# Kernel optimization log

Measured on AMD Instinct MI355X. Metric: run time of the kernel, lower is better.

The kernel has to match this reference:

```python
import jax, jax.numpy as jnp
import numpy as np

B, T, D = 2, 2048, 2048
H, L = 16, 64
Hd = D // H  # 128
SCALE = 1.0 / np.sqrt(L).astype(np.float32)


def apply_rope(q, k, freqs):
    # q, k: [B, T, H, Hd]; freqs: [T, Hd//2] angles (theta)
    cos = jnp.cos(freqs)[None, :, None, :]  # [1,T,1,Hd/2]
    sin = jnp.sin(freqs)[None, :, None, :]

    def rot(t):
        tr = t.reshape(*t.shape[:-1], Hd // 2, 2)
        a, b = tr[..., 0], tr[..., 1]
        return jnp.stack([a * cos - b * sin, a * sin + b * cos], axis=-1).reshape(t.shape)

    return rot(q), rot(k)


def setup_inputs() -> dict:
    key = jax.random.key(0)
    ks = jax.random.split(key, 16)

    def w(k, shape):
        return jax.random.normal(k, shape, jnp.float32) * 0.02

    x = jax.random.normal(ks[0], (B, T, D), jnp.float32)
    # RoPE angles: theta[t, i] = t / 10000^(2i/Hd)
    inv = 1.0 / (10000.0 ** (jnp.arange(0, Hd, 2, dtype=jnp.float32) / Hd))
    freqs = jnp.arange(T, dtype=jnp.float32)[:, None] * inv[None, :]  # [T, Hd/2]
    # additive causal mask
    mask = jnp.where(jnp.tril(jnp.ones((T, T), bool)), 0.0, -1e9).astype(jnp.float32)

    return dict(
        x=x, freqs=freqs, mask=mask,
        Wq=w(ks[1], (D, D)), bq=jnp.zeros((D,), jnp.float32),
        Wk=w(ks[2], (D, D)), bk=jnp.zeros((D,), jnp.float32),
        Wv=w(ks[3], (D, D)), bv=jnp.zeros((D,), jnp.float32),
        Wo=w(ks[4], (D, D)), bo=jnp.zeros((D,), jnp.float32),
        Wcq=w(ks[5], (Hd, L)), bcq=jnp.zeros((L,), jnp.float32),
        Wck=w(ks[6], (Hd, L)), bck=jnp.zeros((L,), jnp.float32),
        Wcv=w(ks[7], (Hd, L)), bcv=jnp.zeros((L,), jnp.float32),
        Wd=w(ks[8], (L, Hd)), bd=jnp.zeros((Hd,), jnp.float32),
    )


def reference(x, freqs, mask, Wq, bq, Wk, bk, Wv, bv, Wo, bo,
              Wcq, bcq, Wck, bck, Wcv, bcv, Wd, bd):
    b, t, d = x.shape
    q = (x @ Wq + bq).reshape(b, t, H, Hd)
    k = (x @ Wk + bk).reshape(b, t, H, Hd)
    v = (x @ Wv + bv).reshape(b, t, H, Hd)

    q, k = apply_rope(q, k, freqs)

    # per-head latent compression [B,T,H,L]
    q_lat = jnp.einsum('bthd,dl->bthl', q, Wcq) + bcq
    k_lat = jnp.einsum('bthd,dl->bthl', k, Wck) + bck
    v_lat = jnp.einsum('bthd,dl->bthl', v, Wcv) + bcv

    scores = jnp.einsum('bthl,bshl->bhts', q_lat, k_lat) * SCALE
    scores = scores + mask[None, None, :, :]
    attn = jax.nn.softmax(scores, axis=-1)

    out = jnp.einsum('bhts,bshl->bthl', attn, v_lat)  # [B,T,H,L]
    out = jnp.einsum('bthl,lk->bthk', out, Wd) + bd    # decompress -> [B,T,H,Hd]
    out = out.reshape(b, t, d)
    return out @ Wo + bo
```

## Files before the change

### kernel.cpp

```cpp
#include <hip/hip_runtime.h>
#include <hip/hip_bf16.h>

static constexpr int Bsz = 2;
static constexpr int Tn  = 2048;
static constexpr int Dn  = 2048;
static constexpr int Hn  = 16;
static constexpr int Ln  = 64;
static constexpr int Hd  = 128;
static constexpr float SL2E = 0.125f * 1.44269504088896f;

typedef short short8 __attribute__((ext_vector_type(8)));
typedef float f32x4 __attribute__((ext_vector_type(4)));
typedef unsigned short ushort8 __attribute__((ext_vector_type(8)));
typedef unsigned short ushort4v __attribute__((ext_vector_type(4)));
typedef _Float16 half8 __attribute__((ext_vector_type(8)));
typedef unsigned short u16;

__device__ inline u16 f16_rne(float f) {
  _Float16 h = (_Float16)f;
  union { _Float16 h; u16 u; } x; x.h = h;
  return x.u;
}
__device__ inline float f16_to_f(u16 u) {
  union { u16 u; _Float16 h; } x; x.u = u;
  return (float)x.h;
}

#define GL(g, l) __builtin_amdgcn_global_load_lds(                     \
    (const __attribute__((address_space(1))) void*)(g),                \
    (__attribute__((address_space(3))) void*)(l), 16, 0, 0)

__global__ void split_h(const float* __restrict__ A, u16* __restrict__ O,
                        int nblk, int Kd) {
  int b = blockIdx.x * 256 + threadIdx.x;
  if (b >= nblk) return;
  int perRow = Kd >> 3;
  int m = b / perRow, gb = b - m * perRow;
  int w = gb >> 2, g = gb & 3;
  const float* src = A + (size_t)m * Kd + (w << 5) + (g << 2);
  float4 v0 = *(const float4*)src;
  float4 v1 = *(const float4*)(src + 16);
  float e[8] = {v0.x, v0.y, v0.z, v0.w, v1.x, v1.y, v1.z, v1.w};
  ushort8 o;
#pragma unroll
  for (int j = 0; j < 8; ++j) o[j] = f16_rne(e[j]);
  *(ushort8*)(O + (size_t)b * 8) = o;
}

__global__ __launch_bounds__(256) void transpose_h2(
    const float* __restrict__ W0, const float* __restrict__ W1,
    u16* __restrict__ T0, u16* __restrict__ T1, int Kd, int Nd) {
  const float* W = blockIdx.z ? W1 : W0;
  u16* Th = blockIdx.z ? T1 : T0;
  __shared__ float t[32][33];
  int k0 = blockIdx.x * 32, n0 = blockIdx.y * 32;
  int i = threadIdx.x;
  {
    int kk = i >> 3, nn = (i & 7) << 2;
    float4 v = *(const float4*)&W[(size_t)(k0 + kk) * Nd + n0 + nn];
    t[kk][nn] = v.x; t[kk][nn + 1] = v.y; t[kk][nn + 2] = v.z; t[kk][nn + 3] = v.w;
  }
  __syncthreads();
  int n = i >> 3, t2 = i & 7;
  int g = t2 >> 1, h = t2 & 1;
  int kbase = h * 16 + g * 4;
  ushort4v o;
#pragma unroll
  for (int j = 0; j < 4; ++j) o[j] = f16_rne(t[kbase + j][n]);
  *(ushort4v*)(Th + (size_t)(n0 + n) * Kd + k0 + t2 * 4) = o;
}

__global__ __launch_bounds__(256) void fold64(
    const float* __restrict__ A, int lda, int a_bx, int a_by,
    const float* __restrict__ B, int ldb, int b_bx, int b_by,
    float* __restrict__ C, int ldc, int c_bx, int c_by) {
  __shared__ float a_lds[64][132];
  __shared__ float b_lds[128][64];
  const int bx = blockIdx.x, by = blockIdx.y, tid = threadIdx.x;
  A += (size_t)bx * a_bx + (size_t)by * a_by;
  B += (size_t)bx * b_bx + (size_t)by * b_by;
  C += (size_t)bx * c_bx + (size_t)by * c_by;
  for (int i = tid; i < 64 * 32; i += 256) {
    int r = i >> 5, c4 = (i & 31) << 2;
    *(float4*)&a_lds[r][c4] = *(const float4*)&A[(size_t)r * lda + c4];
  }
  for (int i = tid; i < 128 * 16; i += 256) {
    int r = i >> 4, c4 = (i & 15) << 2;
    *(float4*)&b_lds[r][c4] = *(const float4*)&B[(size_t)r * ldb + c4];
  }
  __syncthreads();
  const int r = tid >> 2, l0 = (tid & 3) << 4;
  float acc[16] = {};
  for (int k = 0; k < 128; ++k) {
    float av = a_lds[r][k];
    const float* bp = &b_lds[k][l0];
#pragma unroll
    for (int j = 0; j < 16; ++j) acc[j] += av * bp[j];
  }
#pragma unroll
  for (int j4 = 0; j4 < 4; ++j4)
    *(float4*)&C[(size_t)r * ldc + l0 + j4 * 4] = *(float4*)&acc[j4 * 4];
}

__global__ __launch_bounds__(256) void bias_prep(
    const float* __restrict__ bv, const float* __restrict__ Wcv,
    const float* __restrict__ bcv, const float* __restrict__ bd,
    const float* __restrict__ Wo, const float* __restrict__ bo,
    float* __restrict__ bias_vf, float* __restrict__ bias_out) {
  __shared__ float red[4][64];
  if (blockIdx.x == 32) {
    for (int e = threadIdx.x; e < 1024; e += 256) {
      int h = e >> 6, l = e & 63;
      float s = bcv[l];
      for (int j = 0; j < 128; ++j) s += bv[h * 128 + j] * Wcv[j * 64 + l];
      bias_vf[e] = s;
    }
  } else {
    int n0 = blockIdx.x * 64;
    int c = threadIdx.x & 63, g = threadIdx.x >> 6;
    float s = 0.f;
    for (int k = g * 512; k < (g + 1) * 512; ++k)
      s += bd[k & 127] * Wo[(size_t)k * 2048 + n0 + c];
    red[g][c] = s;
    __syncthreads();
    if (g == 0)
      bias_out[n0 + c] = red[0][c] + red[1][c] + red[2][c] + red[3][c] + bo[n0 + c];
  }
}

__global__ __launch_bounds__(512) void gemm_qkv(
    const u16* __restrict__ Af, const u16* __restrict__ Bf,
    u16* __restrict__ cQ, u16* __restrict__ cK, u16* __restrict__ cV,
    const float* __restrict__ bq, const float* __restrict__ bk,
    const float* __restrict__ bvf, int K) {
  __shared__ u16 s[2][2][128 * 64];
  const int tid = threadIdx.x;
  const int lane = tid & 63;
  const int w = tid >> 6;
  const int wr = w >> 2, wc = w & 3;
  const int l15 = lane & 15, lg = lane >> 4;
  const int row0 = blockIdx.y * 128, col0 = blockIdx.x * 128;

  const int sr = tid >> 3, sq = tid & 7;
  const int sg = sq ^ (sr & 7);
  size_t aoff[2], boff[2];
#pragma unroll
  for (int j = 0; j < 2; ++j) {
    aoff[j] = (size_t)(row0 + j * 64 + sr) * K + sg * 8;
    boff[j] = (size_t)(col0 + j * 64 + sr) * K + sg * 8;
  }

  f32x4 acc[4][2];
#pragma unroll
  for (int i2 = 0; i2 < 4; ++i2)
#pragma unroll
    for (int j2 = 0; j2 < 2; ++j2) acc[i2][j2] = (f32x4){0.f, 0.f, 0.f, 0.f};

  int fa[4][2], fb[2][2];
#pragma unroll
  for (int mi = 0; mi < 4; ++mi) {
    int ra = wr * 64 + mi * 16 + l15;
#pragma unroll
    for (int kk = 0; kk < 2; ++kk)
      fa[mi][kk] = ra * 128 + (((kk * 4 + lg) ^ (ra & 7)) << 4);
  }
#pragma unroll
  for (int ni = 0; ni < 2; ++ni) {
    int rb = wc * 32 + ni * 16 + l15;
#pragma unroll
    for (int kk = 0; kk < 2; ++kk)
      fb[ni][kk] = 16384 + rb * 128 + (((kk * 4 + lg) ^ (rb & 7)) << 4);
  }

#pragma unroll
  for (int j = 0; j < 2; ++j) {
    GL(Af + aoff[j], (char*)&s[0][0][0] + j * 8192 + tid * 16);
    GL(Bf + boff[j], (char*)&s[0][1][0] + j * 8192 + tid * 16);
  }
  int cur = 0;
  for (int k0 = 0; k0 < K; k0 += 64) {
    __syncthreads();
    if (k0 + 64 < K) {
      const int nb = cur ^ 1;
#pragma unroll
      for (int j = 0; j < 2; ++j) {
        GL(Af + aoff[j] + k0 + 64, (char*)&s[nb][0][0] + j * 8192 + tid * 16);
        GL(Bf + boff[j] + k0 + 64, (char*)&s[nb][1][0] + j * 8192 + tid * 16);
      }
    }
#pragma unroll
    for (int kk = 0; kk < 2; ++kk) {
      half8 a[4], b[2];
#pragma unroll
      for (int mi = 0; mi < 4; ++mi)
        a[mi] = *(const half8*)((const char*)&s[cur][0][0] + fa[mi][kk]);
#pragma unroll
      for (int ni = 0; ni < 2; ++ni)
        b[ni] = *(const half8*)((const char*)&s[cur][0][0] + fb[ni][kk]);
#pragma unroll
      for (int mi = 0; mi < 4; ++mi)
#pragma unroll
        for (int ni = 0; ni < 2; ++ni)
          acc[mi][ni] = __builtin_amdgcn_mfma_f32_16x16x32_f16(a[mi], b[ni], acc[mi][ni], 0, 0, 0);
    }
    cur ^= 1;
  }
  u16* Cp; const float* bp; int ldc, cl0;
  if (col0 < 2048)      { Cp = cQ; bp = bq;  ldc = 2048; cl0 = col0; }
  else if (col0 < 4096) { Cp = cK; bp = bk;  ldc = 2048; cl0 = col0 - 2048; }
  else                  { Cp = cV; bp = bvf; ldc = 1024; cl0 = col0 - 4096; }
#pragma unroll
  for (int ni = 0; ni < 2; ++ni) {
    int c = cl0 + wc * 32 + ni * 16 + l15;
    float bias = bp[c];
#pragma unroll
    for (int mi = 0; mi < 4; ++mi) {
      int rr = row0 + wr * 64 + mi * 16 + lg * 4;
#pragma unroll
      for (int r = 0; r < 4; ++r)
        Cp[(size_t)(rr + r) * ldc + c] = f16_rne(acc[mi][ni][r] + bias);
    }
  }
}

__global__ __launch_bounds__(512) void gemm_f16(
    const u16* __restrict__ Af, const u16* __restrict__ Bf,
    const float* __restrict__ bias, float* __restrict__ C,
    int M, int N, int K) {
  __shared__ u16 s[2][2][128 * 64];
  const int tid = threadIdx.x;
  const int lane = tid & 63;
  const int w = tid >> 6;
  const int wr = w >> 2, wc = w & 3;
  const int l15 = lane & 15, lg = lane >> 4;
  const int row0 = blockIdx.y * 128, col0 = blockIdx.x * 128;

  const int sr = tid >> 3, sq = tid & 7;
  const int sg = sq ^ (sr & 7);
  size_t aoff[2], boff[2];
#pragma unroll
  for (int j = 0; j < 2; ++j) {
    aoff[j] = (size_t)(row0 + j * 64 + sr) * K + sg * 8;
    boff[j] = (size_t)(col0 + j * 64 + sr) * K + sg * 8;
  }

  f32x4 acc[4][2];
#pragma unroll
  for (int i2 = 0; i2 < 4; ++i2)
#pragma unroll
    for (int j2 = 0; j2 < 2; ++j2) acc[i2][j2] = (f32x4){0.f, 0.f, 0.f, 0.f};

  int fa[4][2], fb[2][2];
#pragma unroll
  for (int mi = 0; mi < 4; ++mi) {
    int ra = wr * 64 + mi * 16 + l15;
#pragma unroll
    for (int kk = 0; kk < 2; ++kk)
      fa[mi][kk] = ra * 128 + (((kk * 4 + lg) ^ (ra & 7)) << 4);
  }
#pragma unroll
  for (int ni = 0; ni < 2; ++ni) {
    int rb = wc * 32 + ni * 16 + l15;
#pragma unroll
    for (int kk = 0; kk < 2; ++kk)
      fb[ni][kk] = 16384 + rb * 128 + (((kk * 4 + lg) ^ (rb & 7)) << 4);
  }

#pragma unroll
  for (int j = 0; j < 2; ++j) {
    GL(Af + aoff[j], (char*)&s[0][0][0] + j * 8192 + tid * 16);
    GL(Bf + boff[j], (char*)&s[0][1][0] + j * 8192 + tid * 16);
  }
  int cur = 0;
  for (int k0 = 0; k0 < K; k0 += 64) {
    __syncthreads();
    if (k0 + 64 < K) {
      const int nb = cur ^ 1;
#pragma unroll
      for (int j = 0; j < 2; ++j) {
        GL(Af + aoff[j] + k0 + 64, (char*)&s[nb][0][0] + j * 8192 + tid * 16);
        GL(Bf + boff[j] + k0 + 64, (char*)&s[nb][1][0] + j * 8192 + tid * 16);
      }
    }
#pragma unroll
    for (int kk = 0; kk < 2; ++kk) {
      half8 a[4], b[2];
#pragma unroll
      for (int mi = 0; mi < 4; ++mi)
        a[mi] = *(const half8*)((const char*)&s[cur][0][0] + fa[mi][kk]);
#pragma unroll
      for (int ni = 0; ni < 2; ++ni)
        b[ni] = *(const half8*)((const char*)&s[cur][0][0] + fb[ni][kk]);
#pragma unroll
      for (int mi = 0; mi < 4; ++mi)
#pragma unroll
        for (int ni = 0; ni < 2; ++ni)
          acc[mi][ni] = __builtin_amdgcn_mfma_f32_16x16x32_f16(a[mi], b[ni], acc[mi][ni], 0, 0, 0);
    }
    cur ^= 1;
  }
#pragma unroll
  for (int ni = 0; ni < 2; ++ni) {
    int c = col0 + wc * 32 + ni * 16 + l15;
    float bv = bias[c];
#pragma unroll
    for (int mi = 0; mi < 4; ++mi) {
      int rr = row0 + wr * 64 + mi * 16 + lg * 4;
#pragma unroll
      for (int r = 0; r < 4; ++r)
        C[(size_t)(rr + r) * N + c] = acc[mi][ni][r] + bv;
    }
  }
}

__global__ __launch_bounds__(256) void compress_qk_mfma(
    const u16* __restrict__ srcQ, const u16* __restrict__ srcK,
    const u16* __restrict__ WcTq, const u16* __restrict__ WcTk,
    const float* __restrict__ bcq, const float* __restrict__ bck,
    const float* __restrict__ freqs,
    u16* __restrict__ dstQ, u16* __restrict__ dstK) {
  const u16* src = blockIdx.z ? srcK : srcQ;
  const u16* WcT = blockIdx.z ? WcTk : WcTq;
  const float* bc = blockIdx.z ? bck : bcq;
  u16* dst = blockIdx.z ? dstK : dstQ;
  __shared__ u16 q_lds[64 * 128];
  __shared__ u16 w_lds[64 * 128];
  const int tid = threadIdx.x;
  const int lane = tid & 63;
  const int w = tid >> 6;
  const int t0 = blockIdx.x * 64;
  const int bh = blockIdx.y, b = bh >> 4, h = bh & 15;

#pragma unroll
  for (int j = 0; j < 4; ++j) {
    int idx = tid + j * 256;
    int row = idx >> 4, slot = idx & 15;
    GL(WcT + (size_t)row * 128 + (size_t)(slot ^ (row & 7)) * 8,
       (char*)w_lds + idx * 16);
  }
  const int r = tid >> 2, seg = tid & 3;
  const u16* qp = src + ((size_t)(b * Tn + t0 + r)) * Dn + h * 128 + seg * 32;
  const float* fp = freqs + (size_t)(t0 + r) * 64 + seg * 16;
  float fr[16];
#pragma unroll
  for (int j = 0; j < 4; ++j) *(float4*)&fr[4 * j] = ((const float4*)fp)[j];
#pragma unroll
  for (int j = 0; j < 8; ++j) {
    ushort4v uv = *(const ushort4v*)(qp + 4 * j);
    float e0 = f16_to_f(uv[0]), e1 = f16_to_f(uv[1]);
    float e2 = f16_to_f(uv[2]), e3 = f16_to_f(uv[3]);
    float s0, c0, s1, c1;
    sincosf(fr[2 * j], &s0, &c0);
    sincosf(fr[2 * j + 1], &s1, &c1);
    ushort4v u;
    u[0] = f16_rne(e0 * c0 - e1 * s0);
    u[1] = f16_rne(e0 * s0 + e1 * c0);
    u[2] = f16_rne(e2 * c1 - e3 * s1);
    u[3] = f16_rne(e2 * s1 + e3 * c1);
    int slot = seg * 4 + (j & 3);
    *(ushort4v*)((char*)q_lds + r * 256 + ((slot ^ (r & 7)) << 4) + (j >> 2) * 8) = u;
  }
  __syncthreads();
  const int l15 = lane & 15, lg = lane >> 4;
  const int arow = w * 16 + l15;
  half8 af[4];
#pragma unroll
  for (int ks = 0; ks < 4; ++ks)
    af[ks] = *(const half8*)((const char*)q_lds + arow * 256 +
                             (((ks * 4 + lg) ^ (arow & 7)) << 4));
  f32x4 acc[4];
#pragma unroll
  for (int ni = 0; ni < 4; ++ni) acc[ni] = (f32x4){0.f, 0.f, 0.f, 0.f};
#pragma unroll
  for (int ni = 0; ni < 4; ++ni) {
    const int brow = ni * 16 + l15;
#pragma unroll
    for (int ks = 0; ks < 4; ++ks) {
      half8 bf = *(const half8*)((const char*)w_lds + brow * 256 +
                                 (((ks * 4 + lg) ^ (brow & 7)) << 4));
      acc[ni] = __builtin_amdgcn_mfma_f32_16x16x32_f16(af[ks], bf, acc[ni], 0, 0, 0);
    }
  }
  __syncthreads();
#pragma unroll
  for (int ni = 0; ni < 4; ++ni) {
    int lat = ni * 16 + l15;
    float bcv = bc[lat];
    int p = (lat & 32) + ((lat >> 2) & 3) * 8 + ((lat >> 4) & 1) * 4 + (lat & 3);
#pragma unroll
    for (int reg = 0; reg < 4; ++reg)
      q_lds[w * 1024 + (lg * 4 + reg) * 64 + p] = f16_rne(acc[ni][reg] + bcv);
  }
  __syncthreads();
#pragma unroll
  for (int j = 0; j < 2; ++j) {
    int idx = tid + j * 256;
    int row = idx >> 3, c8 = idx & 7;
    ushort8 val = *(const ushort8*)&q_lds[row * 64 + c8 * 8];
    *(ushort8*)(dst + ((size_t)bh * Tn + t0 + row) * 64 + c8 * 8) = val;
  }
}

__global__ __launch_bounds__(256) void transpose_v(
    const u16* __restrict__ vlat, u16* __restrict__ vlatT) {
  __shared__ u16 o_lds[64][64];
  const int tid = threadIdx.x;
  const int t0 = blockIdx.x * 64;
  const int bh = blockIdx.y, b = bh >> 4, h = bh & 15;
  const int tt = tid >> 2, lseg = tid & 3;
  const u16* vp = vlat + (size_t)(b * Tn + t0 + tt) * 1024 + h * 64 + lseg * 16;
#pragma unroll
  for (int g = 0; g < 4; ++g) {
    ushort4v u = *(const ushort4v*)(vp + g * 4);
    *(ushort4v*)&o_lds[tt][lseg * 16 + ((g ^ (tt & 3)) << 2)] = u;
  }
  __syncthreads();
  const int lat = tid >> 2, tseg = tid & 3;
  const int tw = tseg >> 1, h4 = tseg & 1;
  u16 vals[16];
#pragma unroll
  for (int i = 0; i < 16; ++i)
    vals[i] = o_lds[tseg * 16 + i][lat ^ ((i & 3) << 2)];
  u16* dp = vlatT + ((size_t)bh * 64 + lat) * Tn + t0 + tw * 32 + h4 * 4;
#pragma unroll
  for (int g = 0; g < 4; ++g) {
    ushort4v u = {vals[g * 4 + 0], vals[g * 4 + 1], vals[g * 4 + 2], vals[g * 4 + 3]};
    *(ushort4v*)(dp + g * 8) = u;
  }
}

__global__ __launch_bounds__(256) void attn_mfma(
    const u16* __restrict__ qlat, const u16* __restrict__ klat,
    const u16* __restrict__ vlatT, u16* __restrict__ oh) {
  __shared__ u16 Ks[64 * 72];
  __shared__ u16 Vs[64 * 72];
  __shared__ u16 Os[64][72];
  const int tid = threadIdx.x;
  const int lane = tid & 63;
  const int w = tid >> 6;
  const int lin = (int)(blockIdx.x + blockIdx.y * gridDim.x);
  const int nchunk = (int)(gridDim.x * gridDim.y) >> 3;
  const int swz = (lin & 7) * nchunk + (lin >> 3);
  const int bh = swz >> 5, b = bh >> 4, h = bh & 15;
  const int q0 = (31 - (swz & 31)) * 64;
  const int qw = q0 + w * 16;
  const u16* ql = qlat + (size_t)bh * Tn * 64;
  const u16* kl = klat + (size_t)bh * Tn * 64;
  const u16* vt = vlatT + (size_t)bh * 64 * Tn;
  const int l15 = lane & 15, lg = lane >> 4;

  half8 qf[2];
#pragma unroll
  for (int ks = 0; ks < 2; ++ks)
    qf[ks] = *(const half8*)(const void*)(ql + (size_t)(qw + l15) * 64 + (ks * 4 + lg) * 8);

  f32x4 accO[4];
#pragma unroll
  for (int mi = 0; mi < 4; ++mi) accO[mi] = (f32x4){0.f, 0.f, 0.f, 0.f};
  float mrow = -1e30f, lrow = 0.f;

  const int srow = tid >> 2, spair = tid & 3;
  u16* ksw = &Ks[srow * 72 + spair * 16];
  u16* vsw = &Vs[srow * 72 + spair * 16];
  const u16* kgp = kl + (size_t)srow * 64 + spair * 16;
  const u16* vgp = vt + (size_t)srow * Tn + spair * 16;

  ushort8 kr0 = *(const ushort8*)(kgp);
  ushort8 kr1 = *(const ushort8*)(kgp + 8);
  ushort8 vr0 = *(const ushort8*)(vgp);
  ushort8 vr1 = *(const ushort8*)(vgp + 8);

  const int ntiles = q0 / 64 + 1;
  for (int kt = 0; kt < ntiles; ++kt) {
    const int k0 = kt * 64;
    __syncthreads();
    *(ushort8*)ksw       = kr0;
    *(ushort8*)(ksw + 8) = kr1;
    *(ushort8*)vsw       = vr0;
    *(ushort8*)(vsw + 8) = vr1;
    __syncthreads();
    {
      int kn = k0 + 64; kn = kn > (int)Tn - 64 ? (int)Tn - 64 : kn;
      kr0 = *(const ushort8*)(kgp + (size_t)kn * 64);
      kr1 = *(const ushort8*)(kgp + (size_t)kn * 64 + 8);
      vr0 = *(const ushort8*)(vgp + kn);
      vr1 = *(const ushort8*)(vgp + kn + 8);
    }
    f32x4 s4[4];
#pragma unroll
    for (int mi = 0; mi < 4; ++mi) s4[mi] = (f32x4){0.f, 0.f, 0.f, 0.f};
    __builtin_amdgcn_s_setprio(1);
#pragma unroll
    for (int ks = 0; ks < 2; ++ks) {
      half8 kf[4];
#pragma unroll
      for (int mi = 0; mi < 4; ++mi)
        kf[mi] = *(const half8*)(const void*)&Ks[(mi * 16 + l15) * 72 + (ks * 4 + lg) * 8];
#pragma unroll
      for (int mi = 0; mi < 4; ++mi)
        s4[mi] = __builtin_amdgcn_mfma_f32_16x16x32_f16(kf[mi], qf[ks], s4[mi], 0, 0, 0);
    }
    __builtin_amdgcn_s_setprio(0);
    const bool needmask = (kt == ntiles - 1);
    const int qidx = qw + l15;
    float p[4][4];
    float tmax = -1e30f;
#pragma unroll
    for (int mi = 0; mi < 4; ++mi)
#pragma unroll
      for (int rr = 0; rr < 4; ++rr) {
        float v = s4[mi][rr] * SL2E;
        if (needmask && (k0 + mi * 16 + lg * 4 + rr > qidx)) v = -1e30f;
        p[mi][rr] = v;
        tmax = fmaxf(tmax, v);
      }
    tmax = fmaxf(tmax, __shfl_xor(tmax, 16));
    tmax = fmaxf(tmax, __shfl_xor(tmax, 32));
    if (!__all(tmax - mrow <= 8.f)) {
      float mnew = fmaxf(mrow, tmax);
      float alpha = exp2f(mrow - mnew);
      lrow *= alpha;
#pragma unroll
      for (int mi = 0; mi < 4; ++mi)
#pragma unroll
        for (int rr = 0; rr < 4; ++rr) accO[mi][rr] *= alpha;
      mrow = mnew;
    }
    float psum = 0.f;
    u16 ph[4][4];
#pragma unroll
    for (int mi = 0; mi < 4; ++mi)
#pragma unroll
      for (int rr = 0; rr < 4; ++rr) {
        float e = exp2f(p[mi][rr] - mrow);
        u16 hb = f16_rne(e);
        psum += f16_to_f(hb);
        ph[mi][rr] = hb;
      }
    psum += __shfl_xor(psum, 16);
    psum += __shfl_xor(psum, 32);
    lrow += psum;
    ushort8 pf[2];
#pragma unroll
    for (int ks = 0; ks < 2; ++ks) {
      ushort8 f;
#pragma unroll
      for (int rr = 0; rr < 4; ++rr) {
        f[rr]     = ph[2 * ks][rr];
        f[4 + rr] = ph[2 * ks + 1][rr];
      }
      pf[ks] = f;
    }
    __builtin_amdgcn_s_setprio(1);
#pragma unroll
    for (int ks = 0; ks < 2; ++ks) {
      half8 vf[4];
#pragma unroll
      for (int mi = 0; mi < 4; ++mi)
        vf[mi] = *(const half8*)(const void*)&Vs[(mi * 16 + l15) * 72 + (ks * 4 + lg) * 8];
#pragma unroll
      for (int mi = 0; mi < 4; ++mi)
        accO[mi] = __builtin_amdgcn_mfma_f32_16x16x32_f16(vf[mi], *(const half8*)&pf[ks], accO[mi], 0, 0, 0);
    }
    __builtin_amdgcn_s_setprio(0);
  }
  __syncthreads();
  {
    float inv = 1.f / lrow;
    int qloc = w * 16 + l15;
#pragma unroll
    for (int mi = 0; mi < 4; ++mi) {
      int pbase = (mi >> 1) * 32 + lg * 8 + (mi & 1) * 4;
      ushort4v u;
#pragma unroll
      for (int rr = 0; rr < 4; ++rr) u[rr] = f16_rne(accO[mi][rr] * inv);
      *(ushort4v*)&Os[qloc][pbase] = u;
    }
  }
  __syncthreads();
  {
    int rid = tid >> 2, seg = tid & 3;
    u16* dstp = oh + ((size_t)(b * Tn + q0 + rid)) * 1024 + h * 64 + seg * 16;
#pragma unroll
    for (int g = 0; g < 2; ++g)
      *(ushort8*)(dstp + g * 8) = *(const ushort8*)&Os[rid][seg * 16 + g * 8];
  }
}

extern "C" void kernel_launch(void* const* d_in, const int* in_sizes, int n_in,
                              void* d_out, int out_size, void* d_ws, size_t ws_size,
                              hipStream_t stream) {
  const float* x     = (const float*)d_in[0];
  const float* freqs = (const float*)d_in[1];
  const float* Wq  = (const float*)d_in[3];  const float* bq  = (const float*)d_in[4];
  const float* Wk  = (const float*)d_in[5];  const float* bk  = (const float*)d_in[6];
  const float* Wv  = (const float*)d_in[7];  const float* bv  = (const float*)d_in[8];
  const float* Wo  = (const float*)d_in[9];  const float* bo  = (const float*)d_in[10];
  const float* Wcq = (const float*)d_in[11]; const float* bcq = (const float*)d_in[12];
  const float* Wck = (const float*)d_in[13]; const float* bck = (const float*)d_in[14];
  const float* Wcv = (const float*)d_in[15]; const float* bcv = (const float*)d_in[16];
  const float* Wd  = (const float*)d_in[17]; const float* bd  = (const float*)d_in[18];
  float* out = (float*)d_out;

  const size_t BT = (size_t)Bsz * Tn;
  const size_t nQ = BT * Dn;
  const size_t nL = BT * Hn * Ln;
  const size_t nWT = (size_t)5120 * 2048;

  char* ws = (char*)d_ws;
  u16* xf   = (u16*)ws;
  u16* WTf  = xf + nQ;
  float* Wvf = (float*)(WTf + nWT);
  u16* Qh   = (u16*)(Wvf + (size_t)2048 * 1024);
  u16* Kh   = Qh + nQ;
  u16* vlat = Kh + nQ;
  float* bias_vf  = (float*)(vlat + (size_t)4096 * 1024);
  float* bias_out = bias_vf + 1024;
  u16* qlat  = (u16*)(bias_out + 2048);
  u16* klat  = qlat + nL;
  u16* vlatT = klat + nL;
  u16* oh = (u16*)(vlatT + nL);
  float* Wdo = (float*)(oh + (size_t)4096 * 1024);
  u16* WdoT = (u16*)(Wdo + (size_t)1024 * 2048);
  u16* WcqT = WdoT + (size_t)2048 * 1024;
  u16* WckT = WcqT + (size_t)64 * 128;

  dim3 blk(256);
  int nblkA = (int)(nQ / 8);

  split_h<<<(nblkA + 255) / 256, blk, 0, stream>>>(x, xf, nblkA, Dn);
  fold64<<<dim3(32, 16), blk, 0, stream>>>(Wv, 2048, 64 * 2048, 128,
                                           Wcv, 64, 0, 0,
                                           Wvf, 1024, 64 * 1024, 64);
  transpose_h2<<<dim3(64, 64, 2), blk, 0, stream>>>(Wq, Wk, WTf,
                                                    WTf + (size_t)2048 * 2048, 2048, 2048);
  transpose_h2<<<dim3(64, 32, 1), blk, 0, stream>>>(Wvf, Wvf, WTf + (size_t)4096 * 2048,
                                                    WTf + (size_t)4096 * 2048, 2048, 1024);
  transpose_h2<<<dim3(4, 2, 2), blk, 0, stream>>>(Wcq, Wck, WcqT, WckT, 128, 64);
  bias_prep<<<33, blk, 0, stream>>>(bv, Wcv, bcv, bd, Wo, bo, bias_vf, bias_out);

  gemm_qkv<<<dim3(40, 32), dim3(512), 0, stream>>>(xf, WTf, Qh, Kh, vlat,
                                                   bq, bk, bias_vf, 2048);

  compress_qk_mfma<<<dim3(Tn / 64, Bsz * Hn, 2), blk, 0, stream>>>(
      Qh, Kh, WcqT, WckT, bcq, bck, freqs, qlat, klat);
  transpose_v<<<dim3(Tn / 64, Bsz * Hn), blk, 0, stream>>>(vlat, vlatT);

  attn_mfma<<<dim3(Tn / 64, Bsz * Hn), blk, 0, stream>>>(qlat, klat, vlatT, oh);

  fold64<<<dim3(32, 16), blk, 0, stream>>>(Wd, 128, 0, 0,
                                           Wo, 2048, 64, 128 * 2048,
                                           Wdo, 2048, 64, 64 * 2048);
  transpose_h2<<<dim3(32, 64, 1), blk, 0, stream>>>(Wdo, Wdo, WdoT, WdoT, 1024, 2048);
  gemm_f16<<<dim3(16, 32), dim3(512), 0, stream>>>(oh, WdoT, bias_out, out, (int)BT, 2048, 1024);
}
```

Measured before the change: 325.5 us.

## Use triple-buffered K=32 tiles with explicit vmcnt waits in GEMM kernels

Both GEMM kernels switch from double-buffered 64-wide K tiles to triple-buffered 32-wide K tiles. The LDS swizzle is adjusted for the narrower tile, and a single barrier per iteration is paired with an explicit s_waitcnt vmcnt(2). This keeps two global-to-LDS loads in flight while computing, to hide memory latency better. In exchange there are twice as many loop iterations and barriers, and each barrier has less MFMA work to amortise it.

After: 333.1 us. +2.3%, slower.

```diff
diff --git a/kernel.cpp b/kernel.cpp
--- a/kernel.cpp
+++ b/kernel.cpp
@@ -133,7 +133,7 @@
     u16* __restrict__ cQ, u16* __restrict__ cK, u16* __restrict__ cV,
     const float* __restrict__ bq, const float* __restrict__ bk,
     const float* __restrict__ bvf, int K) {
-  __shared__ u16 s[2][2][128 * 64];
+  __shared__ u16 s[3][2][128 * 32];
   const int tid = threadIdx.x;
   const int lane = tid & 63;
   const int w = tid >> 6;
@@ -141,14 +141,11 @@
   const int l15 = lane & 15, lg = lane >> 4;
   const int row0 = blockIdx.y * 128, col0 = blockIdx.x * 128;
 
-  const int sr = tid >> 3, sq = tid & 7;
-  const int sg = sq ^ (sr & 7);
-  size_t aoff[2], boff[2];
-#pragma unroll
-  for (int j = 0; j < 2; ++j) {
-    aoff[j] = (size_t)(row0 + j * 64 + sr) * K + sg * 8;
-    boff[j] = (size_t)(col0 + j * 64 + sr) * K + sg * 8;
-  }
+  const int sr = tid >> 2, sq = tid & 3;
+  const int sg = sq ^ ((sr >> 1) & 3);
+  const size_t aoff = (size_t)(row0 + sr) * K + sg * 8;
+  const size_t boff = (size_t)(col0 + sr) * K + sg * 8;
+  const int ldst = tid * 16;
 
   f32x4 acc[4][2];
 #pragma unroll
@@ -156,54 +153,47 @@
 #pragma unroll
     for (int j2 = 0; j2 < 2; ++j2) acc[i2][j2] = (f32x4){0.f, 0.f, 0.f, 0.f};
 
-  int fa[4][2], fb[2][2];
+  int fa[4], fb[2];
 #pragma unroll
   for (int mi = 0; mi < 4; ++mi) {
     int ra = wr * 64 + mi * 16 + l15;
-#pragma unroll
-    for (int kk = 0; kk < 2; ++kk)
-      fa[mi][kk] = ra * 128 + (((kk * 4 + lg) ^ (ra & 7)) << 4);
+    fa[mi] = ra * 64 + ((lg ^ ((ra >> 1) & 3)) << 4);
   }
 #pragma unroll
   for (int ni = 0; ni < 2; ++ni) {
     int rb = wc * 32 + ni * 16 + l15;
-#pragma unroll
-    for (int kk = 0; kk < 2; ++kk)
-      fb[ni][kk] = 16384 + rb * 128 + (((kk * 4 + lg) ^ (rb & 7)) << 4);
-  }
-
-#pragma unroll
-  for (int j = 0; j < 2; ++j) {
-    GL(Af + aoff[j], (char*)&s[0][0][0] + j * 8192 + tid * 16);
-    GL(Bf + boff[j], (char*)&s[0][1][0] + j * 8192 + tid * 16);
-  }
-  int cur = 0;
-  for (int k0 = 0; k0 < K; k0 += 64) {
-    __syncthreads();
-    if (k0 + 64 < K) {
-      const int nb = cur ^ 1;
-#pragma unroll
-      for (int j = 0; j < 2; ++j) {
-        GL(Af + aoff[j] + k0 + 64, (char*)&s[nb][0][0] + j * 8192 + tid * 16);
-        GL(Bf + boff[j] + k0 + 64, (char*)&s[nb][1][0] + j * 8192 + tid * 16);
-      }
-    }
-#pragma unroll
-    for (int kk = 0; kk < 2; ++kk) {
-      half8 a[4], b[2];
-#pragma unroll
-      for (int mi = 0; mi < 4; ++mi)
-        a[mi] = *(const half8*)((const char*)&s[cur][0][0] + fa[mi][kk]);
+    fb[ni] = rb * 64 + ((lg ^ ((rb >> 1) & 3)) << 4);
+  }
+
+  const int NT = K >> 5;
+  GL(Af + aoff,      (char*)&s[0][0][0] + ldst);
+  GL(Bf + boff,      (char*)&s[0][1][0] + ldst);
+  GL(Af + aoff + 32, (char*)&s[1][0][0] + ldst);
+  GL(Bf + boff + 32, (char*)&s[1][1][0] + ldst);
+  int cb = 0;
+  for (int kt = 0; kt < NT; ++kt) {
+    __builtin_amdgcn_sched_barrier(0);
+    if (kt + 1 < NT) asm volatile("s_waitcnt vmcnt(2)" ::: "memory");
+    else             asm volatile("s_waitcnt vmcnt(0)" ::: "memory");
+    __builtin_amdgcn_s_barrier();
+    if (kt + 2 < NT) {
+      int nb = cb - 1; if (nb < 0) nb = 2;
+      GL(Af + aoff + (size_t)(kt + 2) * 32, (char*)&s[nb][0][0] + ldst);
+      GL(Bf + boff + (size_t)(kt + 2) * 32, (char*)&s[nb][1][0] + ldst);
+    }
+    half8 a[4], b[2];
+#pragma unroll
+    for (int mi = 0; mi < 4; ++mi)
+      a[mi] = *(const half8*)((const char*)&s[cb][0][0] + fa[mi]);
+#pragma unroll
+    for (int ni = 0; ni < 2; ++ni)
+      b[ni] = *(const half8*)((const char*)&s[cb][1][0] + fb[ni]);
+#pragma unroll
+    for (int mi = 0; mi < 4; ++mi)
 #pragma unroll
       for (int ni = 0; ni < 2; ++ni)
-        b[ni] = *(const half8*)((const char*)&s[cur][0][0] + fb[ni][kk]);
-#pragma unroll
-      for (int mi = 0; mi < 4; ++mi)
-#pragma unroll
-        for (int ni = 0; ni < 2; ++ni)
-          acc[mi][ni] = __builtin_amdgcn_mfma_f32_16x16x32_f16(a[mi], b[ni], acc[mi][ni], 0, 0, 0);
-    }
-    cur ^= 1;
+        acc[mi][ni] = __builtin_amdgcn_mfma_f32_16x16x32_f16(a[mi], b[ni], acc[mi][ni], 0, 0, 0);
+    cb = cb + 1; if (cb == 3) cb = 0;
   }
   u16* Cp; const float* bp; int ldc, cl0;
   if (col0 < 2048)      { Cp = cQ; bp = bq;  ldc = 2048; cl0 = col0; }
@@ -227,7 +217,7 @@
     const u16* __restrict__ Af, const u16* __restrict__ Bf,
     const float* __restrict__ bias, float* __restrict__ C,
     int M, int N, int K) {
-  __shared__ u16 s[2][2][128 * 64];
+  __shared__ u16 s[3][2][128 * 32];
   const int tid = threadIdx.x;
   const int lane = tid & 63;
   const int w = tid >> 6;
@@ -235,14 +225,11 @@
   const int l15 = lane & 15, lg = lane >> 4;
   const int row0 = blockIdx.y * 128, col0 = blockIdx.x * 128;
 
-  const int sr = tid >> 3, sq = tid & 7;
-  const int sg = sq ^ (sr & 7);
-  size_t aoff[2], boff[2];
-#pragma unroll
-  for (int j = 0; j < 2; ++j) {
-    aoff[j] = (size_t)(row0 + j * 64 + sr) * K + sg * 8;
-    boff[j] = (size_t)(col0 + j * 64 + sr) * K + sg * 8;
-  }
+  const int sr = tid >> 2, sq = tid & 3;
+  const int sg = sq ^ ((sr >> 1) & 3);
+  const size_t aoff = (size_t)(row0 + sr) * K + sg * 8;
+  const size_t boff = (size_t)(col0 + sr) * K + sg * 8;
+  const int ldst = tid * 16;
 
   f32x4 acc[4][2];
 #pragma unroll
@@ -250,54 +237,47 @@
 #pragma unroll
     for (int j2 = 0; j2 < 2; ++j2) acc[i2][j2] = (f32x4){0.f, 0.f, 0.f, 0.f};
 
-  int fa[4][2], fb[2][2];
+  int fa[4], fb[2];
 #pragma unroll
   for (int mi = 0; mi < 4; ++mi) {
     int ra = wr * 64 + mi * 16 + l15;
-#pragma unroll
-    for (int kk = 0; kk < 2; ++kk)
-      fa[mi][kk] = ra * 128 + (((kk * 4 + lg) ^ (ra & 7)) << 4);
+    fa[mi] = ra * 64 + ((lg ^ ((ra >> 1) & 3)) << 4);
   }
 #pragma unroll
   for (int ni = 0; ni < 2; ++ni) {
     int rb = wc * 32 + ni * 16 + l15;
-#pragma unroll
-    for (int kk = 0; kk < 2; ++kk)
-      fb[ni][kk] = 16384 + rb * 128 + (((kk * 4 + lg) ^ (rb & 7)) << 4);
-  }
-
-#pragma unroll
-  for (int j = 0; j < 2; ++j) {
-    GL(Af + aoff[j], (char*)&s[0][0][0] + j * 8192 + tid * 16);
-    GL(Bf + boff[j], (char*)&s[0][1][0] + j * 8192 + tid * 16);
-  }
-  int cur = 0;
-  for (int k0 = 0; k0 < K; k0 += 64) {
-    __syncthreads();
-    if (k0 + 64 < K) {
-      const int nb = cur ^ 1;
-#pragma unroll
-      for (int j = 0; j < 2; ++j) {
-        GL(Af + aoff[j] + k0 + 64, (char*)&s[nb][0][0] + j * 8192 + tid * 16);
-        GL(Bf + boff[j] + k0 + 64, (char*)&s[nb][1][0] + j * 8192 + tid * 16);
-      }
-    }
-#pragma unroll
-    for (int kk = 0; kk < 2; ++kk) {
-      half8 a[4], b[2];
-#pragma unroll
-      for (int mi = 0; mi < 4; ++mi)
-        a[mi] = *(const half8*)((const char*)&s[cur][0][0] + fa[mi][kk]);
+    fb[ni] = rb * 64 + ((lg ^ ((rb >> 1) & 3)) << 4);
+  }
+
+  const int NT = K >> 5;
+  GL(Af + aoff,      (char*)&s[0][0][0] + ldst);
+  GL(Bf + boff,      (char*)&s[0][1][0] + ldst);
+  GL(Af + aoff + 32, (char*)&s[1][0][0] + ldst);
+  GL(Bf + boff + 32, (char*)&s[1][1][0] + ldst);
+  int cb = 0;
+  for (int kt = 0; kt < NT; ++kt) {
+    __builtin_amdgcn_sched_barrier(0);
+    if (kt + 1 < NT) asm volatile("s_waitcnt vmcnt(2)" ::: "memory");
+    else             asm volatile("s_waitcnt vmcnt(0)" ::: "memory");
+    __builtin_amdgcn_s_barrier();
+    if (kt + 2 < NT) {
+      int nb = cb - 1; if (nb < 0) nb = 2;
+      GL(Af + aoff + (size_t)(kt + 2) * 32, (char*)&s[nb][0][0] + ldst);
+      GL(Bf + boff + (size_t)(kt + 2) * 32, (char*)&s[nb][1][0] + ldst);
+    }
+    half8 a[4], b[2];
+#pragma unroll
+    for (int mi = 0; mi < 4; ++mi)
+      a[mi] = *(const half8*)((const char*)&s[cb][0][0] + fa[mi]);
+#pragma unroll
+    for (int ni = 0; ni < 2; ++ni)
+      b[ni] = *(const half8*)((const char*)&s[cb][1][0] + fb[ni]);
+#pragma unroll
+    for (int mi = 0; mi < 4; ++mi)
 #pragma unroll
       for (int ni = 0; ni < 2; ++ni)
-        b[ni] = *(const half8*)((const char*)&s[cur][0][0] + fb[ni][kk]);
-#pragma unroll
-      for (int mi = 0; mi < 4; ++mi)
-#pragma unroll
-        for (int ni = 0; ni < 2; ++ni)
-          acc[mi][ni] = __builtin_amdgcn_mfma_f32_16x16x32_f16(a[mi], b[ni], acc[mi][ni], 0, 0, 0);
-    }
-    cur ^= 1;
+        acc[mi][ni] = __builtin_amdgcn_mfma_f32_16x16x32_f16(a[mi], b[ni], acc[mi][ni], 0, 0, 0);
+    cb = cb + 1; if (cb == 3) cb = 0;
   }
 #pragma unroll
   for (int ni = 0; ni < 2; ++ni) {
```
